# Optimization experiments

Hardware: AMD Instinct MI355X
Metric: run time of the kernel (lower is better)

Reference implementation:

```python
import jax, jax.numpy as jnp
import numpy as np

B, C, H, W = 128, 3, 256, 256


def setup_inputs() -> dict:
    key = jax.random.key(0)
    k1, k2, k3, k4 = jax.random.split(key, 4)
    img = jax.random.uniform(k1, (B, C, H, W), jnp.float32)
    # init in the module: rot=PI, trans=0, scale=1, shear=0; add small noise
    rot = jnp.pi + 0.5 * jax.random.normal(k2, (B, 1), jnp.float32)
    trans = 0.1 * jax.random.normal(k3, (B, 2), jnp.float32)
    scale = jnp.ones((B, 1), jnp.float32)
    shear = 0.1 * jax.random.normal(k4, (B, 2), jnp.float32)
    return {"img": img, "rot": rot, "trans": trans, "scale": scale, "shear": shear}


def _theta(rot, trans, scale, shear):
    # 2x3 affine matrix per sample: A = scale * R(rot) @ Shear, last col = trans
    r = rot[:, 0]
    s = scale[:, 0]
    c, sn = jnp.cos(r), jnp.sin(r)
    shx, shy = shear[:, 0], shear[:, 1]
    a00 = s * (c - sn * shy)
    a01 = s * (c * shx - sn)
    a10 = s * (sn + c * shy)
    a11 = s * (sn * shx + c)
    row0 = jnp.stack([a00, a01, trans[:, 0]], axis=-1)  # [B,3]
    row1 = jnp.stack([a10, a11, trans[:, 1]], axis=-1)  # [B,3]
    return jnp.stack([row0, row1], axis=1)  # [B,2,3]


def _affine_grid(theta, Hc, Wc):
    # normalized coords, align_corners=False convention
    ys = (2.0 * (jnp.arange(Hc, dtype=jnp.float32) + 0.5) / Hc) - 1.0
    xs = (2.0 * (jnp.arange(Wc, dtype=jnp.float32) + 0.5) / Wc) - 1.0
    gx, gy = jnp.meshgrid(xs, ys)  # [H,W]
    base = jnp.stack([gx, gy, jnp.ones_like(gx)], axis=-1)  # [H,W,3]
    return jnp.einsum('bij,hwj->bhwi', theta, base)  # [B,H,W,2] -> (x,y)


def _grid_sample(img, grid):
    # bilinear, zeros padding, align_corners=False
    Bc, Cc, Hc, Wc = img.shape
    ix = ((grid[..., 0] + 1.0) * Wc - 1.0) / 2.0
    iy = ((grid[..., 1] + 1.0) * Hc - 1.0) / 2.0
    x0 = jnp.floor(ix); y0 = jnp.floor(iy)
    x1 = x0 + 1.0; y1 = y0 + 1.0
    wx1 = ix - x0; wx0 = 1.0 - wx1
    wy1 = iy - y0; wy0 = 1.0 - wy1
    flat = img.reshape(Bc, Cc, Hc * Wc)

    def gather(xi, yi, w):
        valid = (xi >= 0) & (xi <= Wc - 1) & (yi >= 0) & (yi <= Hc - 1)
        xc = jnp.clip(xi, 0, Wc - 1).astype(jnp.int32)
        yc = jnp.clip(yi, 0, Hc - 1).astype(jnp.int32)
        idx = (yc * Wc + xc).reshape(Bc, 1, -1)  # [B,1,H*W]
        vals = jnp.take_along_axis(flat, idx, axis=2)  # [B,C,H*W]
        wm = (w * valid.astype(w.dtype)).reshape(Bc, 1, -1)
        return vals * wm

    out = (gather(x0, y0, wx0 * wy0) + gather(x1, y0, wx1 * wy0)
           + gather(x0, y1, wx0 * wy1) + gather(x1, y1, wx1 * wy1))
    return out.reshape(Bc, Cc, Hc, Wc)


def reference(img, rot, trans, scale, shear):
    theta = _theta(rot, trans, scale, shear)
    grid = _affine_grid(theta, img.shape[2], img.shape[3])
    return _grid_sample(img, grid)
```

## Files before the change

kernel.cpp:

```cpp
#include <hip/hip_runtime.h>
#include <math.h>

#define BATCH 128
#define CHAN  3
#define IMH   256
#define IMW   256
#define NXCD  8
#define TW    32
#define TH    16

#define BH_T   42
#define NC_MAX 44
#define ROWSTR 132

__global__ __launch_bounds__(256) void affine_sample_kernel(
        const float* __restrict__ img,
        const float* __restrict__ rot,
        const float* __restrict__ trans,
        const float* __restrict__ scale,
        const float* __restrict__ shear,
        float* __restrict__ out) {
    __shared__ float tile[BH_T * ROWSTR];

    const int NBLK = BATCH * (IMH / TH) * (IMW / TW);
    const int p = blockIdx.x;
    const int L = (p & (NXCD - 1)) * (NBLK / NXCD) + (p >> 3);

    const int b  = L >> 7;
    const int tl = L & 127;
    const int w0 = (tl & 7) * TW;
    const int h0 = (tl >> 3) * TH;

    const float r   = rot[b];
    const float s   = scale[b];
    const float shx = shear[2 * b + 0];
    const float shy = shear[2 * b + 1];
    const float txr = trans[2 * b + 0];
    const float tyr = trans[2 * b + 1];
    const float c  = __cosf(r);
    const float sn = __sinf(r);
    const float a00 = s * (c - sn * shy);
    const float a01 = s * (c * shx - sn);
    const float a10 = s * (sn + c * shy);
    const float a11 = s * (sn * shx + c);
    const float g0x = 1.0f / (float)IMW - 1.0f;
    const float g0y = 1.0f / (float)IMH - 1.0f;
    const float Cx = ((a00 * g0x + a01 * g0y + txr + 1.0f) * (float)IMW - 1.0f) * 0.5f;
    const float Cy = ((a10 * g0x + a11 * g0y + tyr + 1.0f) * (float)IMH - 1.0f) * 0.5f;
    const float hx = 15.5f * fabsf(a00) + 7.5f * fabsf(a01);
    const float hy = 15.5f * fabsf(a10) + 7.5f * fabsf(a11);

    const float ixc = Cx + a00 * ((float)w0 + 15.5f) + a01 * ((float)h0 + 7.5f);
    const float iyc = Cy + a10 * ((float)w0 + 15.5f) + a11 * ((float)h0 + 7.5f);
    const int xlu = (int)floorf(ixc - hx);
    const int xhu = (int)floorf(ixc + hx) + 1;
    const int ylu = (int)floorf(iyc - hy);
    const int yhu = (int)floorf(iyc + hy) + 1;
    const bool interior = (xlu >= 1) & (xhu <= IMW - 2) & (ylu >= 1) & (yhu <= IMH - 2);

    const int x_lo = min(max(xlu, 0), IMW - 1);
    const int x_hi = min(max(xhu, 0), IMW - 1);
    const int y_lo = min(max(ylu, 0), IMH - 1);
    const int y_hi = min(max(yhu, 0), IMH - 1);
    const int xs  = (x_lo - 1) & ~1;
    const int ys  = y_lo - 1;
    const int ncs = x_hi + 2 - xs;
    const int nrs = y_hi + 2 - ys;

    const int t  = threadIdx.x;
    const int wq = w0 + (t & 31);
    const int hq = h0 + ((t >> 5) << 1);
    const float ixa = Cx + a00 * (float)wq + a01 * (float)hq;
    const float iya = Cy + a10 * (float)wq + a11 * (float)hq;
    const float2 ixv = {ixa, ixa + a01};
    const float2 iyv = {iya, iya + a11};
    const float2 x0fv = {floorf(ixv.x), floorf(ixv.y)};
    const float2 y0fv = {floorf(iyv.x), floorf(iyv.y)};
    const float2 wx1v = ixv - x0fv;
    const float2 wy1v = iyv - y0fv;
    const float2 onev = {1.0f, 1.0f};
    const float2 wx0v = onev - wx1v;
    const float2 wy0v = onev - wy1v;
    float2 w00v = wx0v * wy0v;
    float2 w10v = wx1v * wy0v;
    float2 w01v = wx0v * wy1v;
    float2 w11v = wx1v * wy1v;
    if (!interior) {
        const bool vx0a = (x0fv.x >= 0.0f) & (x0fv.x <= (float)(IMW - 1));
        const bool vx1a = (x0fv.x >= -1.0f) & (x0fv.x <= (float)(IMW - 2));
        const bool vy0a = (y0fv.x >= 0.0f) & (y0fv.x <= (float)(IMH - 1));
        const bool vy1a = (y0fv.x >= -1.0f) & (y0fv.x <= (float)(IMH - 2));
        if (!(vx0a && vy0a)) w00v.x = 0.0f;
        if (!(vx1a && vy0a)) w10v.x = 0.0f;
        if (!(vx0a && vy1a)) w01v.x = 0.0f;
        if (!(vx1a && vy1a)) w11v.x = 0.0f;
        const bool vx0b = (x0fv.y >= 0.0f) & (x0fv.y <= (float)(IMW - 1));
        const bool vx1b = (x0fv.y >= -1.0f) & (x0fv.y <= (float)(IMW - 2));
        const bool vy0b = (y0fv.y >= 0.0f) & (y0fv.y <= (float)(IMH - 1));
        const bool vy1b = (y0fv.y >= -1.0f) & (y0fv.y <= (float)(IMH - 2));
        if (!(vx0b && vy0b)) w00v.y = 0.0f;
        if (!(vx1b && vy0b)) w10v.y = 0.0f;
        if (!(vx0b && vy1b)) w01v.y = 0.0f;
        if (!(vx1b && vy1b)) w11v.y = 0.0f;
    }
    const int x0ia = (int)x0fv.x, y0ia = (int)y0fv.x;
    const int x0ib = (int)x0fv.y, y0ib = (int)y0fv.y;

    const int plane = IMH * IMW;
    const int obase = (b * CHAN) * plane + hq * IMW + wq;
    const float* ibase = img + (size_t)(b * CHAN) * plane;

    if (ncs <= NC_MAX && nrs <= BH_T) {
        const int lx2 = (t & 31) << 1;
        const int lyr = t >> 5;
        const int nrd = (nrs + 7) >> 3;
        const bool wcol = lx2 < ncs;
        if (interior) {
            const float* colp = ibase + (xs + lx2);
            for (int rr = 0; rr < nrd; ++rr) {
                const int dy = (rr << 3) + lyr;
                if (wcol & (dy < nrs)) {
                    const float* src = colp + (ys + dy) * IMW;
                    const float2 v0 = *(const float2*)(src);
                    const float2 v1 = *(const float2*)(src + plane);
                    const float2 v2 = *(const float2*)(src + 2 * plane);
                    float* dst = &tile[dy * ROWSTR + lx2 * 3];
                    dst[0] = v0.x; dst[1] = v1.x; dst[2] = v2.x;
                    dst[3] = v0.y; dst[4] = v1.y; dst[5] = v2.y;
                }
            }
        } else {
            const int xg = min(max(xs + lx2, 0), IMW - 2);
            for (int rr = 0; rr < nrd; ++rr) {
                const int dy = (rr << 3) + lyr;
                if (wcol & (dy < nrs)) {
                    const int yg = min(max(ys + dy, 0), IMH - 1);
                    const float* src = ibase + yg * IMW + xg;
                    const float2 v0 = *(const float2*)(src);
                    const float2 v1 = *(const float2*)(src + plane);
                    const float2 v2 = *(const float2*)(src + 2 * plane);
                    float* dst = &tile[dy * ROWSTR + lx2 * 3];
                    dst[0] = v0.x; dst[1] = v1.x; dst[2] = v2.x;
                    dst[3] = v0.y; dst[4] = v1.y; dst[5] = v2.y;
                }
            }
        }
        __syncthreads();

        int rxa, rya, rxb, ryb;
        if (interior) {
            rxa = x0ia - xs;  rya = y0ia - ys;
            rxb = x0ib - xs;  ryb = y0ib - ys;
        } else {
            rxa = min(max(x0ia - xs, 0), ncs - 2);
            rya = min(max(y0ia - ys, 0), nrs - 2);
            rxb = min(max(x0ib - xs, 0), ncs - 2);
            ryb = min(max(y0ib - ys, 0), nrs - 2);
        }
        const float* tpa = &tile[rya * ROWSTR + rxa * 3];
        const float* tpb = &tile[ryb * ROWSTR + rxb * 3];
#pragma unroll
        for (int cc = 0; cc < CHAN; ++cc) {
            const float2 t00 = {tpa[cc],              tpb[cc]};
            const float2 t10 = {tpa[cc + 3],          tpb[cc + 3]};
            const float2 t01 = {tpa[cc + ROWSTR],     tpb[cc + ROWSTR]};
            const float2 t11 = {tpa[cc + ROWSTR + 3], tpb[cc + ROWSTR + 3]};
            const float2 v = w00v * t00 + w10v * t10 + w01v * t01 + w11v * t11;
            out[obase + cc * plane]       = v.x;
            out[obase + cc * plane + IMW] = v.y;
        }
    } else {
        const int x0ca = min(max(x0ia, 0), IMW - 1);
        const int x1ca = min(max(x0ia + 1, 0), IMW - 1);
        const int y0ca = min(max(y0ia, 0), IMH - 1);
        const int y1ca = min(max(y0ia + 1, 0), IMH - 1);
        const int x0cb = min(max(x0ib, 0), IMW - 1);
        const int x1cb = min(max(x0ib + 1, 0), IMW - 1);
        const int y0cb = min(max(y0ib, 0), IMH - 1);
        const int y1cb = min(max(y0ib + 1, 0), IMH - 1);
#pragma unroll
        for (int cc = 0; cc < CHAN; ++cc) {
            const float* p2 = ibase + cc * plane;
            const float va = w00v.x * p2[y0ca * IMW + x0ca] + w10v.x * p2[y0ca * IMW + x1ca]
                           + w01v.x * p2[y1ca * IMW + x0ca] + w11v.x * p2[y1ca * IMW + x1ca];
            const float vb = w00v.y * p2[y0cb * IMW + x0cb] + w10v.y * p2[y0cb * IMW + x1cb]
                           + w01v.y * p2[y1cb * IMW + x0cb] + w11v.y * p2[y1cb * IMW + x1cb];
            out[obase + cc * plane]       = va;
            out[obase + cc * plane + IMW] = vb;
        }
    }
}

extern "C" void kernel_launch(void* const* d_in, const int* in_sizes, int n_in,
                              void* d_out, int out_size, void* d_ws, size_t ws_size,
                              hipStream_t stream) {
    const float* img   = (const float*)d_in[0];
    const float* rot   = (const float*)d_in[1];
    const float* trans = (const float*)d_in[2];
    const float* scale = (const float*)d_in[3];
    const float* shear = (const float*)d_in[4];
    float* out = (float*)d_out;

    const int nblocks = BATCH * (IMH / TH) * (IMW / TW);
    affine_sample_kernel<<<nblocks, 256, 0, stream>>>(img, rot, trans, scale,
                                                      shear, out);
}
```

Baseline: 42.75 us.

## Stage image tiles into LDS via direct global-to-LDS loads with planar layout

```diff
diff --git a/kernel.cpp b/kernel.cpp
--- a/kernel.cpp
+++ b/kernel.cpp
@@ -9,9 +9,11 @@
 #define TW    32
 #define TH    16
 
-#define BH_T   42
+#define BH_T   40
 #define NC_MAX 44
-#define ROWSTR 132
+#define CH_STR 1792
+
+typedef unsigned int u32;
 
 __global__ __launch_bounds__(256) void affine_sample_kernel(
         const float* __restrict__ img,
@@ -20,7 +22,7 @@
         const float* __restrict__ scale,
         const float* __restrict__ shear,
         float* __restrict__ out) {
-    __shared__ float tile[BH_T * ROWSTR];
+    __shared__ float tile[CHAN * CH_STR];
 
     const int NBLK = BATCH * (IMH / TH) * (IMW / TW);
     const int p = blockIdx.x;
@@ -111,25 +113,35 @@
     const float* ibase = img + (size_t)(b * CHAN) * plane;
 
     if (ncs <= NC_MAX && nrs <= BH_T) {
-        const int lx2 = (t & 31) << 1;
-        const int lyr = t >> 5;
-        const int nrd = (nrs + 7) >> 3;
-        const bool wcol = lx2 < ncs;
-        if (interior) {
-            const float* colp = ibase + (xs + lx2);
-            for (int rr = 0; rr < nrd; ++rr) {
-                const int dy = (rr << 3) + lyr;
-                if (wcol & (dy < nrs)) {
-                    const float* src = colp + (ys + dy) * IMW;
-                    const float2 v0 = *(const float2*)(src);
-                    const float2 v1 = *(const float2*)(src + plane);
-                    const float2 v2 = *(const float2*)(src + 2 * plane);
-                    float* dst = &tile[dy * ROWSTR + lx2 * 3];
-                    dst[0] = v0.x; dst[1] = v1.x; dst[2] = v2.x;
-                    dst[3] = v0.y; dst[4] = v1.y; dst[5] = v2.y;
+        const bool dma = (b > 0) & (b < BATCH - 1);
+        if (dma) {
+            const int wid  = t >> 6;
+            const int lane = t & 63;
+            int idx = (wid << 8) + (lane << 2);
+            int row = idx / 44;
+            int col = idx - row * 44;
+            const int Nch  = (nrs * 44 + 255) >> 8;
+            const int soff = ys * IMW + xs;
+            for (int j = wid; j < Nch; j += 4) {
+                const int off = soff + row * IMW + col;
+#pragma unroll
+                for (int cc = 0; cc < CHAN; ++cc) {
+                    const float* gp = ibase + cc * plane + off;
+                    __builtin_amdgcn_global_load_lds(
+                        (const __attribute__((address_space(1))) u32*)(const void*)gp,
+                        (__attribute__((address_space(3))) u32*)(void*)
+                            &tile[cc * CH_STR + (j << 8)],
+                        16, 0, 0);
                 }
+                row += 23; col += 12;
+                const int wr = (col >= 44) ? 1 : 0;
+                col -= wr * 44; row += wr;
             }
         } else {
+            const int lx2 = (t & 31) << 1;
+            const int lyr = t >> 5;
+            const int nrd = (nrs + 7) >> 3;
+            const bool wcol = lx2 < ncs;
             const int xg = min(max(xs + lx2, 0), IMW - 2);
             for (int rr = 0; rr < nrd; ++rr) {
                 const int dy = (rr << 3) + lyr;
@@ -139,9 +151,10 @@
                     const float2 v0 = *(const float2*)(src);
                     const float2 v1 = *(const float2*)(src + plane);
                     const float2 v2 = *(const float2*)(src + 2 * plane);
-                    float* dst = &tile[dy * ROWSTR + lx2 * 3];
-                    dst[0] = v0.x; dst[1] = v1.x; dst[2] = v2.x;
-                    dst[3] = v0.y; dst[4] = v1.y; dst[5] = v2.y;
+                    float* d0 = &tile[dy * NC_MAX + lx2];
+                    d0[0] = v0.x;               d0[1] = v0.y;
+                    d0[CH_STR] = v1.x;          d0[CH_STR + 1] = v1.y;
+                    d0[2 * CH_STR] = v2.x;      d0[2 * CH_STR + 1] = v2.y;
                 }
             }
         }
@@ -157,14 +170,16 @@
             rxb = min(max(x0ib - xs, 0), ncs - 2);
             ryb = min(max(y0ib - ys, 0), nrs - 2);
         }
-        const float* tpa = &tile[rya * ROWSTR + rxa * 3];
-        const float* tpb = &tile[ryb * ROWSTR + rxb * 3];
+        const int la = rya * NC_MAX + rxa;
+        const int lb = ryb * NC_MAX + rxb;
 #pragma unroll
         for (int cc = 0; cc < CHAN; ++cc) {
-            const float2 t00 = {tpa[cc],              tpb[cc]};
-            const float2 t10 = {tpa[cc + 3],          tpb[cc + 3]};
-            const float2 t01 = {tpa[cc + ROWSTR],     tpb[cc + ROWSTR]};
-            const float2 t11 = {tpa[cc + ROWSTR + 3], tpb[cc + ROWSTR + 3]};
+            const float* pa = &tile[cc * CH_STR + la];
+            const float* pb = &tile[cc * CH_STR + lb];
+            const float2 t00 = {pa[0],          pb[0]};
+            const float2 t10 = {pa[1],          pb[1]};
+            const float2 t01 = {pa[NC_MAX],     pb[NC_MAX]};
+            const float2 t11 = {pa[NC_MAX + 1], pb[NC_MAX + 1]};
             const float2 v = w00v * t00 + w10v * t10 + w01v * t01 + w11v * t11;
             out[obase + cc * plane]       = v.x;
             out[obase + cc * plane + IMW] = v.y;
```

After: 38.87 us. 9.1% less time.
